# Performance work log

Hardware: AMD Instinct MI355X
Metric: run time of the kernel (lower is better)

Reference implementation:

```python
import jax, jax.numpy as jnp
import numpy as np
import math

B, H, S, D = 4, 16, 2048, 64

def setup_inputs() -> dict:
    key = jax.random.key(0)
    kq, kk, kv, km = jax.random.split(key, 4)
    query = jax.random.normal(kq, (B, H, S, D), dtype=jnp.float32)
    k = jax.random.normal(kk, (B, H, S, D), dtype=jnp.float32)
    value = jax.random.normal(kv, (B, H, S, D), dtype=jnp.float32)
    mask = jax.random.randint(km, (1, 1, S, S), 0, 2) == 1  # True = masked
    return {"query": query, "key": k, "value": value, "mask": mask}

def reference(query, key, value, mask):
    # scores: [B,H,S,S]
    scale = 1.0 / math.sqrt(key.shape[-1])
    scores = jnp.einsum('bhqd,bhkd->bhqk', query, key) * scale
    scores = jnp.where(mask, -jnp.inf, scores)
    probs = jax.nn.softmax(scores, axis=-1)
    out = jnp.einsum('bhqk,bhkd->bhqd', probs, value)
    return out
```

## Files before the change

### kernel.cpp

```cpp
#include <hip/hip_runtime.h>
#include <hip/hip_bf16.h>
#include <stdint.h>

#define BHN 64
#define SEQ 2048
#define DH  64

typedef unsigned short u16;
typedef __attribute__((ext_vector_type(8))) short bf16x8;
typedef __attribute__((ext_vector_type(16))) float f32x16;

__device__ inline u16 f2bf(float x){
  union { float f; uint32_t u; } a; a.f = x;
  uint32_t u = a.u;
  uint32_t lsb = (u >> 16) & 1u;
  u += 0x7FFFu + lsb;
  return (u16)(u >> 16);
}

__device__ inline float fast_exp2(float x){
#if __has_builtin(__builtin_amdgcn_exp2f)
  return __builtin_amdgcn_exp2f(x);
#else
  float r; asm("v_exp_f32 %0, %1" : "=v"(r) : "v"(x)); return r;
#endif
}

__device__ inline void gload_lds16(const void* g, void* l){
  __builtin_amdgcn_global_load_lds(
      (const __attribute__((address_space(1))) void*)g,
      (__attribute__((address_space(3))) void*)l, 16, 0, 0);
}


__global__ __launch_bounds__(256) void build_tiles(const float* __restrict__ kf,
                                                   const float* __restrict__ vf,
                                                   u16* __restrict__ tiles){
  __shared__ float sVf[64][65];
  int head = blockIdx.x >> 5;
  int kt   = blockIdx.x & 31;
  int k0   = kt * 64;
  int t = threadIdx.x;

  {
    int r = t >> 2;
    int dseg = (t & 3) * 16;
    const float* src = vf + ((int64_t)(head*SEQ + k0 + r))*DH + dseg;
    #pragma unroll
    for (int j = 0; j < 16; j += 4){
      float4 v = *(const float4*)(src + j);
      sVf[r][dseg+j+0] = v.x; sVf[r][dseg+j+1] = v.y;
      sVf[r][dseg+j+2] = v.z; sVf[r][dseg+j+3] = v.w;
    }
  }

  u16* outb = tiles + ((size_t)(head*32 + kt) << 13);

  #pragma unroll
  for (int i = 0; i < 2; i++){
    int cid = i*256 + t;
    int f = cid >> 6;
    int l = cid & 63;
    int kh = f >> 2, ds = f & 3;
    int row = k0 + kh*32 + (l & 31);
    int dstart = ds*16 + (l >> 5)*8;
    const float* src = kf + ((int64_t)(head*SEQ + row))*DH + dstart;
    float4 a = *(const float4*)(src);
    float4 b = *(const float4*)(src + 4);
    union { u16 h[8]; uint4 v; } pk;
    pk.h[0]=f2bf(a.x); pk.h[1]=f2bf(a.y); pk.h[2]=f2bf(a.z); pk.h[3]=f2bf(a.w);
    pk.h[4]=f2bf(b.x); pk.h[5]=f2bf(b.y); pk.h[6]=f2bf(b.z); pk.h[7]=f2bf(b.w);
    *(uint4*)(outb + f*512 + l*8) = pk.v;
  }

  __syncthreads();

  #pragma unroll
  for (int i = 0; i < 2; i++){
    int cid = i*256 + t;
    int g = cid >> 6;
    int l = cid & 63;
    int oh = g >> 2, ks = g & 3;
    int d  = oh*32 + (l & 31);
    int kk = ks*16 + (l >> 5)*8;
    union { u16 h[8]; uint4 v; } pk;
    #pragma unroll
    for (int j = 0; j < 8; j++) pk.h[j] = f2bf(sVf[kk+j][d]);
    *(uint4*)(outb + (8+g)*512 + l*8) = pk.v;
  }
}

__global__ __launch_bounds__(256) void pack_mask(const void* __restrict__ mraw,
                                                 uint32_t* __restrict__ mkp){
  __shared__ int sflag;
  int t = threadIdx.x;
  const uint32_t* m32 = (const uint32_t*)mraw;
  if (t == 0) sflag = 0;
  __syncthreads();
  if (t < 64){
    uint32_t v = m32[t] | m32[t+64] | m32[t+128] | m32[t+192];
    if (v > 1u) atomicOr(&sflag, 1);
  }
  __syncthreads();
  bool isbool = (sflag != 0);
  int idx = blockIdx.x*256 + t;
  int row = idx >> 6;
  int wd  = idx & 63;
  uint32_t bits = 0;
  if (isbool){
    const uint8_t* mb = (const uint8_t*)mraw + (int64_t)row*SEQ + wd*32;
    uint4 a = ((const uint4*)mb)[0];
    uint4 b = ((const uint4*)mb)[1];
    uint32_t words[8] = {a.x,a.y,a.z,a.w,b.x,b.y,b.z,b.w};
    #pragma unroll
    for (int i = 0; i < 32; i++){
      int kl = (i&3) + 8*((i>>2)&3) + 4*(i>>4);
      uint32_t byte = (words[kl>>2] >> (8*(kl&3))) & 0xFFu;
      bits |= (byte ? 0u : 1u) << i;
    }
  } else {
    const uint32_t* mi = m32 + (int64_t)row*SEQ + wd*32;
    uint32_t words[32];
    #pragma unroll
    for (int j = 0; j < 32; j += 4){
      uint4 v = *(const uint4*)(mi + j);
      words[j+0]=v.x; words[j+1]=v.y; words[j+2]=v.z; words[j+3]=v.w;
    }
    #pragma unroll
    for (int i = 0; i < 32; i++){
      int kl = (i&3) + 8*((i>>2)&3) + 4*(i>>4);
      bits |= (words[kl] ? 0u : 1u) << i;
    }
  }
  mkp[((size_t)(wd >> 1)*SEQ + row)*2 + (wd & 1)] = bits;
}


__global__ __launch_bounds__(256, 4) void attn_mfma(
    const float* __restrict__ qf, const u16* __restrict__ tiles,
    const uint32_t* __restrict__ mkp, float* __restrict__ out)
{
  __shared__ __align__(16) char lds[2*16384 + 512];

  int bid = blockIdx.x;
  int logical = (bid & 7)*128 + (bid >> 3);
  int head = logical >> 4;
  int q0   = (logical & 15) * 128;

  int t  = threadIdx.x;
  int w  = t >> 6;
  int l  = t & 63;
  int l31 = l & 31;
  int hi  = l >> 5;
  int hi16 = hi << 4;

  const float QS = 0.125f * 1.4426950408889634f;
  bf16x8 qfr[4];
  {
    const float* qrow = qf + ((size_t)(head*SEQ + q0 + w*32 + l31))*DH + hi*8;
    #pragma unroll
    for (int ds = 0; ds < 4; ds++){
      float4 a = *(const float4*)(qrow + ds*16);
      float4 b = *(const float4*)(qrow + ds*16 + 4);
      uint32_t u0, u1, u2, u3;
      asm("v_cvt_pk_bf16_f32 %0, %1, %2" : "=v"(u0) : "v"(a.x*QS), "v"(a.y*QS));
      asm("v_cvt_pk_bf16_f32 %0, %1, %2" : "=v"(u1) : "v"(a.z*QS), "v"(a.w*QS));
      asm("v_cvt_pk_bf16_f32 %0, %1, %2" : "=v"(u2) : "v"(b.x*QS), "v"(b.y*QS));
      asm("v_cvt_pk_bf16_f32 %0, %1, %2" : "=v"(u3) : "v"(b.z*QS), "v"(b.w*QS));
      union { uint32_t u[4]; bf16x8 h; } pk_;
      pk_.u[0]=u0; pk_.u[1]=u1; pk_.u[2]=u2; pk_.u[3]=u3;
      qfr[ds] = pk_.h;
    }
  }

  const uint2* mptr = (const uint2*)mkp + (q0 + w*32 + l31);

  const char* tb = (const char*)tiles + ((size_t)head << 19) + w*4096 + l*16;
  char* dwave = lds + w*4096;

  f32x16 O0 = {0,0,0,0,0,0,0,0,0,0,0,0,0,0,0,0};
  f32x16 O1 = {0,0,0,0,0,0,0,0,0,0,0,0,0,0,0,0};
  float ls0 = 0.f, ls1 = 0.f;

  const char* ldsL = lds + l*16;

  auto STAGE = [&](int kt64, int bufoff){
    const char* s_ = tb + ((size_t)kt64 << 14);
    char* d_ = dwave + bufoff;
    gload_lds16(s_,        d_);
    gload_lds16(s_ + 1024, d_ + 1024);
    gload_lds16(s_ + 2048, d_ + 2048);
    gload_lds16(s_ + 3072, d_ + 3072);
  };

  STAGE(0, 0);
  uint2 mw2 = *mptr; mptr += SEQ;
  __syncthreads();

  int cur = 0;
  for (int kt = 0; kt < 32; kt++){
    uint2 mw2n = mw2;
    if (kt < 31){
      STAGE(kt+1, cur ^ 16384);
      mw2n = *mptr; mptr += SEQ;
    }

    const char* lb = ldsL + cur;

    #pragma unroll
    for (int g = 0; g < 2; g++){
      uint32_t wsh = (g ? mw2.y : mw2.x) >> hi16;

      f32x16 c = {0,0,0,0,0,0,0,0,0,0,0,0,0,0,0,0};
      __builtin_amdgcn_s_setprio(1);
      #pragma unroll
      for (int ds = 0; ds < 4; ds++){
        bf16x8 kfr = *(const bf16x8*)(lb + (4*g + ds)*1024);
        c = __builtin_amdgcn_mfma_f32_32x32x16_bf16(kfr, qfr[ds], c, 0, 0, 0);
      }
      __builtin_amdgcn_s_setprio(0);

      float p[16];
      #pragma unroll
      for (int r = 0; r < 16; r++){
        float pe = fast_exp2(c[r]);
        int32_t km;
        asm("v_bfe_i32 %0, %1, %2, 1" : "=v"(km) : "v"(wsh), "n"(r));
        p[r] = __uint_as_float(__float_as_uint(pe) & (uint32_t)km);
      }
      #pragma unroll
      for (int r = 0; r < 8; r++){ ls0 += p[r]; ls1 += p[r+8]; }

      bf16x8 pa0, pa1;
      {
        uint32_t A0, A1, B0, B1;
        asm("v_cvt_pk_bf16_f32 %0, %1, %2" : "=v"(A0) : "v"(p[0]), "v"(p[1]));
        asm("v_cvt_pk_bf16_f32 %0, %1, %2" : "=v"(A1) : "v"(p[2]), "v"(p[3]));
        asm("v_cvt_pk_bf16_f32 %0, %1, %2" : "=v"(B0) : "v"(p[4]), "v"(p[5]));
        asm("v_cvt_pk_bf16_f32 %0, %1, %2" : "=v"(B1) : "v"(p[6]), "v"(p[7]));
        asm("v_permlane32_swap_b32 %0, %1" : "+v"(A0), "+v"(B0));
        asm("v_permlane32_swap_b32 %0, %1" : "+v"(A1), "+v"(B1));
        union { uint32_t u[4]; bf16x8 h; } pk_;
        pk_.u[0] = A0; pk_.u[1] = A1; pk_.u[2] = B0; pk_.u[3] = B1;
        pa0 = pk_.h;
      }
      {
        uint32_t A0, A1, B0, B1;
        asm("v_cvt_pk_bf16_f32 %0, %1, %2" : "=v"(A0) : "v"(p[8]),  "v"(p[9]));
        asm("v_cvt_pk_bf16_f32 %0, %1, %2" : "=v"(A1) : "v"(p[10]), "v"(p[11]));
        asm("v_cvt_pk_bf16_f32 %0, %1, %2" : "=v"(B0) : "v"(p[12]), "v"(p[13]));
        asm("v_cvt_pk_bf16_f32 %0, %1, %2" : "=v"(B1) : "v"(p[14]), "v"(p[15]));
        asm("v_permlane32_swap_b32 %0, %1" : "+v"(A0), "+v"(B0));
        asm("v_permlane32_swap_b32 %0, %1" : "+v"(A1), "+v"(B1));
        union { uint32_t u[4]; bf16x8 h; } pk_;
        pk_.u[0] = A0; pk_.u[1] = A1; pk_.u[2] = B0; pk_.u[3] = B1;
        pa1 = pk_.h;
      }

      __builtin_amdgcn_s_setprio(1);
      {
        bf16x8 v00 = *(const bf16x8*)(lb + (8  + 2*g)*1024);
        bf16x8 v01 = *(const bf16x8*)(lb + (9  + 2*g)*1024);
        bf16x8 v10 = *(const bf16x8*)(lb + (12 + 2*g)*1024);
        bf16x8 v11 = *(const bf16x8*)(lb + (13 + 2*g)*1024);
        O0 = __builtin_amdgcn_mfma_f32_32x32x16_bf16(pa0, v00, O0, 0, 0, 0);
        O0 = __builtin_amdgcn_mfma_f32_32x32x16_bf16(pa1, v01, O0, 0, 0, 0);
        O1 = __builtin_amdgcn_mfma_f32_32x32x16_bf16(pa0, v10, O1, 0, 0, 0);
        O1 = __builtin_amdgcn_mfma_f32_32x32x16_bf16(pa1, v11, O1, 0, 0, 0);
      }
      __builtin_amdgcn_s_setprio(0);
    }

    mw2 = mw2n;
    __syncthreads();
    cur ^= 16384;
  }

  float lt = ls0 + ls1;
  {
    uint32_t a = __float_as_uint(lt), b = a;
    asm("v_permlane32_swap_b32 %0, %1" : "+v"(a), "+v"(b));
    lt = __uint_as_float(a) + __uint_as_float(b);
  }
  float* sInv = (float*)(lds + 32768);
  if (hi == 0) sInv[w*32 + l31] = 1.0f / lt;
  float* obase = out + ((size_t)(head*SEQ + q0 + w*32))*DH + l31;
  #pragma unroll
  for (int r = 0; r < 16; r++){
    int qr = (r&3) + 8*(r>>2) + 4*hi;
    float inv = sInv[w*32 + qr];
    obase[(size_t)qr*DH]      = O0[r] * inv;
    obase[(size_t)qr*DH + 32] = O1[r] * inv;
  }
}


__global__ __launch_bounds__(256) void attn_naive(
    const float* __restrict__ qf, const float* __restrict__ kf,
    const float* __restrict__ vf, const void* __restrict__ mraw,
    float* __restrict__ out)
{
  __shared__ float sq[64];
  __shared__ float sS[SEQ];
  __shared__ float redM[4], redS[4];
  __shared__ float sO[4][64];
  __shared__ int sflag;

  int bid = blockIdx.x;
  int bh = bid >> 11;
  int q  = bid & 2047;
  int t  = threadIdx.x;
  const uint32_t* m32 = (const uint32_t*)mraw;
  if (t == 0) sflag = 0;
  __syncthreads();
  if (t < 64){
    uint32_t v = m32[t] | m32[t+64] | m32[t+128] | m32[t+192];
    if (v > 1u) atomicOr(&sflag, 1);
  }
  if (t < 64) sq[t] = qf[((int64_t)bh*SEQ + q)*DH + t] * (0.125f*1.4426950408889634f);
  __syncthreads();
  bool isbool = (sflag != 0);

  float lmax = -3e38f;
  for (int k = t; k < SEQ; k += 256){
    bool masked = isbool ? (((const uint8_t*)mraw)[(int64_t)q*SEQ + k] != 0)
                         : (m32[(int64_t)q*SEQ + k] != 0);
    float s = -3e38f;
    if (!masked){
      const float* krow = kf + ((int64_t)bh*SEQ + k)*DH;
      float acc = 0.f;
      for (int d = 0; d < 64; d++) acc += sq[d]*krow[d];
      s = acc;
    }
    sS[k] = s;
    lmax = fmaxf(lmax, s);
  }
  for (int o = 32; o >= 1; o >>= 1) lmax = fmaxf(lmax, __shfl_xor(lmax, o));
  if ((t & 63) == 0) redM[t >> 6] = lmax;
  __syncthreads();
  float m = fmaxf(fmaxf(redM[0], redM[1]), fmaxf(redM[2], redM[3]));
  float lsum = 0.f;
  for (int k = t; k < SEQ; k += 256){
    float p = exp2f(sS[k] - m);
    sS[k] = p;
    lsum += p;
  }
  for (int o = 32; o >= 1; o >>= 1) lsum += __shfl_xor(lsum, o);
  if ((t & 63) == 0) redS[t >> 6] = lsum;
  __syncthreads();
  float lden = redS[0] + redS[1] + redS[2] + redS[3];

  float o = 0.f;
  int d = t & 63;
  int c = t >> 6;
  for (int k = c*512; k < (c+1)*512; k++)
    o += sS[k] * vf[((int64_t)bh*SEQ + k)*DH + d];
  sO[c][d] = o;
  __syncthreads();
  if (t < 64){
    float r = (sO[0][t] + sO[1][t] + sO[2][t] + sO[3][t]) / lden;
    out[((int64_t)bh*SEQ + q)*DH + t] = r;
  }
}


extern "C" void kernel_launch(void* const* d_in, const int* in_sizes, int n_in,
                              void* d_out, int out_size, void* d_ws, size_t ws_size,
                              hipStream_t stream)
{
  const float* qf = (const float*)d_in[0];
  const float* kf = (const float*)d_in[1];
  const float* vf = (const float*)d_in[2];
  const void*  mraw = d_in[3];
  float* out = (float*)d_out;

  size_t tilesB = (size_t)BHN*32*16384;
  size_t need = tilesB + (size_t)SEQ*64*4 + 256;
  if (ws_size >= need){
    u16* tiles = (u16*)d_ws;
    uint32_t* mkp = (uint32_t*)((char*)d_ws + tilesB);
    hipLaunchKernelGGL(build_tiles, dim3(2048), dim3(256), 0, stream, kf, vf, tiles);
    hipLaunchKernelGGL(pack_mask,   dim3(512),  dim3(256), 0, stream, mraw, mkp);
    hipLaunchKernelGGL(attn_mfma,   dim3(1024), dim3(256), 0, stream, qf, tiles, mkp, out);
  } else {
    hipLaunchKernelGGL(attn_naive, dim3(BHN*SEQ), dim3(256), 0, stream, qf, kf, vf, mraw, out);
  }
}
```

Measured before the change: 112.3 us.

## Fold mask into MFMA accumulator init, sum rows via MFMA, relax barriers

The score accumulator now starts at -128 for masked positions and 0 otherwise, so the QK MFMA adds the mask bias and the per-element bitmask AND after exp2 goes away. Row sums are produced by two extra MFMAs per group against a vector of bf16 ones, replacing the scalar adds, the cross-lane reduction and the LDS reciprocal buffer. The __syncthreads calls become an explicit vmcnt wait plus raw s_barrier, with prefetch issued unconditionally (the last iteration reloads a tile it does not need). The trade-off is more MFMA work per tile in exchange for fewer VALU ops, and masking now relies on exp2 of a -128 bias underflowing to near zero.

```diff
diff --git a/kernel.cpp b/kernel.cpp
--- a/kernel.cpp
+++ b/kernel.cpp
@@ -140,7 +140,7 @@
     const float* __restrict__ qf, const u16* __restrict__ tiles,
     const uint32_t* __restrict__ mkp, float* __restrict__ out)
 {
-  __shared__ __align__(16) char lds[2*16384 + 512];
+  __shared__ __align__(16) char lds[2*16384];
 
   int bid = blockIdx.x;
   int logical = (bid & 7)*128 + (bid >> 3);
@@ -173,14 +173,21 @@
     }
   }
 
-  const uint2* mptr = (const uint2*)mkp + (q0 + w*32 + l31);
+  bf16x8 ones;
+  {
+    union { uint32_t u[4]; bf16x8 h; } o_;
+    o_.u[0]=o_.u[1]=o_.u[2]=o_.u[3]=0x3F803F80u;
+    ones = o_.h;
+  }
+
+  const uint2* mbase = (const uint2*)mkp + (q0 + w*32 + l31);
 
   const char* tb = (const char*)tiles + ((size_t)head << 19) + w*4096 + l*16;
   char* dwave = lds + w*4096;
 
-  f32x16 O0 = {0,0,0,0,0,0,0,0,0,0,0,0,0,0,0,0};
-  f32x16 O1 = {0,0,0,0,0,0,0,0,0,0,0,0,0,0,0,0};
-  float ls0 = 0.f, ls1 = 0.f;
+  f32x16 O0   = {0,0,0,0,0,0,0,0,0,0,0,0,0,0,0,0};
+  f32x16 O1   = {0,0,0,0,0,0,0,0,0,0,0,0,0,0,0,0};
+  f32x16 Osum = {0,0,0,0,0,0,0,0,0,0,0,0,0,0,0,0};
 
   const char* ldsL = lds + l*16;
 
@@ -194,24 +201,35 @@
   };
 
   STAGE(0, 0);
-  uint2 mw2 = *mptr; mptr += SEQ;
-  __syncthreads();
+  asm volatile("" ::: "memory");
+  uint2 mw2 = *mbase;
 
   int cur = 0;
+  #pragma unroll 1
   for (int kt = 0; kt < 32; kt++){
-    uint2 mw2n = mw2;
-    if (kt < 31){
-      STAGE(kt+1, cur ^ 16384);
-      mw2n = *mptr; mptr += SEQ;
-    }
+    int nt = (kt < 31) ? (kt + 1) : 31;
+    STAGE(nt, cur ^ 16384);
+    asm volatile("" ::: "memory");
+    uint2 mnext = mbase[(size_t)nt*SEQ];
+
+    asm volatile("s_waitcnt vmcnt(6)" ::: "memory");
+    __builtin_amdgcn_s_barrier();
+    asm volatile("" ::: "memory");
 
     const char* lb = ldsL + cur;
 
     #pragma unroll
     for (int g = 0; g < 2; g++){
-      uint32_t wsh = (g ? mw2.y : mw2.x) >> hi16;
-
-      f32x16 c = {0,0,0,0,0,0,0,0,0,0,0,0,0,0,0,0};
+      uint32_t nsh = ~((g ? mw2.y : mw2.x) >> hi16);
+
+      f32x16 c;
+      #pragma unroll
+      for (int r = 0; r < 16; r++){
+        int32_t km;
+        asm("v_bfe_i32 %0, %1, %2, 1" : "=v"(km) : "v"(nsh), "n"(r));
+        c[r] = __uint_as_float((uint32_t)km & 0xC3000000u);
+      }
+
       __builtin_amdgcn_s_setprio(1);
       #pragma unroll
       for (int ds = 0; ds < 4; ds++){
@@ -222,14 +240,7 @@
 
       float p[16];
       #pragma unroll
-      for (int r = 0; r < 16; r++){
-        float pe = fast_exp2(c[r]);
-        int32_t km;
-        asm("v_bfe_i32 %0, %1, %2, 1" : "=v"(km) : "v"(wsh), "n"(r));
-        p[r] = __uint_as_float(__float_as_uint(pe) & (uint32_t)km);
-      }
-      #pragma unroll
-      for (int r = 0; r < 8; r++){ ls0 += p[r]; ls1 += p[r+8]; }
+      for (int r = 0; r < 16; r++) p[r] = fast_exp2(c[r]);
 
       bf16x8 pa0, pa1;
       {
@@ -263,32 +274,29 @@
         bf16x8 v01 = *(const bf16x8*)(lb + (9  + 2*g)*1024);
         bf16x8 v10 = *(const bf16x8*)(lb + (12 + 2*g)*1024);
         bf16x8 v11 = *(const bf16x8*)(lb + (13 + 2*g)*1024);
-        O0 = __builtin_amdgcn_mfma_f32_32x32x16_bf16(pa0, v00, O0, 0, 0, 0);
-        O0 = __builtin_amdgcn_mfma_f32_32x32x16_bf16(pa1, v01, O0, 0, 0, 0);
-        O1 = __builtin_amdgcn_mfma_f32_32x32x16_bf16(pa0, v10, O1, 0, 0, 0);
-        O1 = __builtin_amdgcn_mfma_f32_32x32x16_bf16(pa1, v11, O1, 0, 0, 0);
+        O0   = __builtin_amdgcn_mfma_f32_32x32x16_bf16(pa0, v00, O0, 0, 0, 0);
+        O0   = __builtin_amdgcn_mfma_f32_32x32x16_bf16(pa1, v01, O0, 0, 0, 0);
+        O1   = __builtin_amdgcn_mfma_f32_32x32x16_bf16(pa0, v10, O1, 0, 0, 0);
+        O1   = __builtin_amdgcn_mfma_f32_32x32x16_bf16(pa1, v11, O1, 0, 0, 0);
+        Osum = __builtin_amdgcn_mfma_f32_32x32x16_bf16(pa0, ones, Osum, 0, 0, 0);
+        Osum = __builtin_amdgcn_mfma_f32_32x32x16_bf16(pa1, ones, Osum, 0, 0, 0);
       }
       __builtin_amdgcn_s_setprio(0);
     }
 
-    mw2 = mw2n;
-    __syncthreads();
+    asm volatile("" ::: "memory");
+    __builtin_amdgcn_s_barrier();
+    asm volatile("" ::: "memory");
+
+    mw2 = mnext;
     cur ^= 16384;
   }
 
-  float lt = ls0 + ls1;
-  {
-    uint32_t a = __float_as_uint(lt), b = a;
-    asm("v_permlane32_swap_b32 %0, %1" : "+v"(a), "+v"(b));
-    lt = __uint_as_float(a) + __uint_as_float(b);
-  }
-  float* sInv = (float*)(lds + 32768);
-  if (hi == 0) sInv[w*32 + l31] = 1.0f / lt;
   float* obase = out + ((size_t)(head*SEQ + q0 + w*32))*DH + l31;
   #pragma unroll
   for (int r = 0; r < 16; r++){
     int qr = (r&3) + 8*(r>>2) + 4*hi;
-    float inv = sInv[w*32 + qr];
+    float inv = 1.0f / Osum[r];
     obase[(size_t)qr*DH]      = O0[r] * inv;
     obase[(size_t)qr*DH + 32] = O1[r] * inv;
   }
```

After: 114.0 us. No clear change (+1.5%).

## Fold mask into MFMA accumulator init and interleave both score tiles with waitcnt pipelining

Applied to the files above, without the earlier changes.

The mask is no longer applied after exp2. Each score accumulator is seeded with a large negative bias (0xC3000000, about -128) for masked positions, so exp2 underflows to zero and the per-element AND after the exponent goes away. The two QK^T MFMA chains now issue back to back before the softmax and PV stages, so the second tile's MFMAs overlap the first tile's exp. __syncthreads is replaced by an explicit vmcnt wait and raw barriers, with unconditional prefetch (the last tile is reloaded redundantly). This risks correctness if the -128 bias does not fully zero a masked entry, and it raises register pressure from holding two accumulators.

```diff
diff --git a/kernel.cpp b/kernel.cpp
--- a/kernel.cpp
+++ b/kernel.cpp
@@ -173,7 +173,7 @@
     }
   }
 
-  const uint2* mptr = (const uint2*)mkp + (q0 + w*32 + l31);
+  const uint2* mbase = (const uint2*)mkp + (q0 + w*32 + l31);
 
   const char* tb = (const char*)tiles + ((size_t)head << 19) + w*4096 + l*16;
   char* dwave = lds + w*4096;
@@ -193,86 +193,122 @@
     gload_lds16(s_ + 3072, d_ + 3072);
   };
 
+  auto SMPACK = [&](f32x16& c, bf16x8& pa0, bf16x8& pa1){
+    float p[16];
+    #pragma unroll
+    for (int r = 0; r < 16; r++) p[r] = fast_exp2(c[r]);
+    #pragma unroll
+    for (int r = 0; r < 8; r++){ ls0 += p[r]; ls1 += p[r+8]; }
+    {
+      uint32_t A0, A1, B0, B1;
+      asm("v_cvt_pk_bf16_f32 %0, %1, %2" : "=v"(A0) : "v"(p[0]), "v"(p[1]));
+      asm("v_cvt_pk_bf16_f32 %0, %1, %2" : "=v"(A1) : "v"(p[2]), "v"(p[3]));
+      asm("v_cvt_pk_bf16_f32 %0, %1, %2" : "=v"(B0) : "v"(p[4]), "v"(p[5]));
+      asm("v_cvt_pk_bf16_f32 %0, %1, %2" : "=v"(B1) : "v"(p[6]), "v"(p[7]));
+      asm("v_permlane32_swap_b32 %0, %1" : "+v"(A0), "+v"(B0));
+      asm("v_permlane32_swap_b32 %0, %1" : "+v"(A1), "+v"(B1));
+      union { uint32_t u[4]; bf16x8 h; } pk_;
+      pk_.u[0] = A0; pk_.u[1] = A1; pk_.u[2] = B0; pk_.u[3] = B1;
+      pa0 = pk_.h;
+    }
+    {
+      uint32_t A0, A1, B0, B1;
+      asm("v_cvt_pk_bf16_f32 %0, %1, %2" : "=v"(A0) : "v"(p[8]),  "v"(p[9]));
+      asm("v_cvt_pk_bf16_f32 %0, %1, %2" : "=v"(A1) : "v"(p[10]), "v"(p[11]));
+      asm("v_cvt_pk_bf16_f32 %0, %1, %2" : "=v"(B0) : "v"(p[12]), "v"(p[13]));
+      asm("v_cvt_pk_bf16_f32 %0, %1, %2" : "=v"(B1) : "v"(p[14]), "v"(p[15]));
+      asm("v_permlane32_swap_b32 %0, %1" : "+v"(A0), "+v"(B0));
+      asm("v_permlane32_swap_b32 %0, %1" : "+v"(A1), "+v"(B1));
+      union { uint32_t u[4]; bf16x8 h; } pk_;
+      pk_.u[0] = A0; pk_.u[1] = A1; pk_.u[2] = B0; pk_.u[3] = B1;
+      pa1 = pk_.h;
+    }
+  };
+
   STAGE(0, 0);
-  uint2 mw2 = *mptr; mptr += SEQ;
-  __syncthreads();
+  asm volatile("" ::: "memory");
+  uint2 mw2 = *mbase;
 
   int cur = 0;
+  #pragma unroll 1
   for (int kt = 0; kt < 32; kt++){
-    uint2 mw2n = mw2;
-    if (kt < 31){
-      STAGE(kt+1, cur ^ 16384);
-      mw2n = *mptr; mptr += SEQ;
-    }
+    int nt = (kt < 31) ? (kt + 1) : 31;
+    STAGE(nt, cur ^ 16384);
+    asm volatile("" ::: "memory");
+    uint2 mnext = mbase[(size_t)nt*SEQ];
+
+    asm volatile("s_waitcnt vmcnt(6)" ::: "memory");
+    __builtin_amdgcn_s_barrier();
+    asm volatile("" ::: "memory");
 
     const char* lb = ldsL + cur;
-
-    #pragma unroll
-    for (int g = 0; g < 2; g++){
-      uint32_t wsh = (g ? mw2.y : mw2.x) >> hi16;
-
-      f32x16 c = {0,0,0,0,0,0,0,0,0,0,0,0,0,0,0,0};
-      __builtin_amdgcn_s_setprio(1);
-      #pragma unroll
-      for (int ds = 0; ds < 4; ds++){
-        bf16x8 kfr = *(const bf16x8*)(lb + (4*g + ds)*1024);
-        c = __builtin_amdgcn_mfma_f32_32x32x16_bf16(kfr, qfr[ds], c, 0, 0, 0);
-      }
-      __builtin_amdgcn_s_setprio(0);
-
-      float p[16];
-      #pragma unroll
-      for (int r = 0; r < 16; r++){
-        float pe = fast_exp2(c[r]);
-        int32_t km;
-        asm("v_bfe_i32 %0, %1, %2, 1" : "=v"(km) : "v"(wsh), "n"(r));
-        p[r] = __uint_as_float(__float_as_uint(pe) & (uint32_t)km);
-      }
-      #pragma unroll
-      for (int r = 0; r < 8; r++){ ls0 += p[r]; ls1 += p[r+8]; }
-
-      bf16x8 pa0, pa1;
-      {
-        uint32_t A0, A1, B0, B1;
-        asm("v_cvt_pk_bf16_f32 %0, %1, %2" : "=v"(A0) : "v"(p[0]), "v"(p[1]));
-        asm("v_cvt_pk_bf16_f32 %0, %1, %2" : "=v"(A1) : "v"(p[2]), "v"(p[3]));
-        asm("v_cvt_pk_bf16_f32 %0, %1, %2" : "=v"(B0) : "v"(p[4]), "v"(p[5]));
-        asm("v_cvt_pk_bf16_f32 %0, %1, %2" : "=v"(B1) : "v"(p[6]), "v"(p[7]));
-        asm("v_permlane32_swap_b32 %0, %1" : "+v"(A0), "+v"(B0));
-        asm("v_permlane32_swap_b32 %0, %1" : "+v"(A1), "+v"(B1));
-        union { uint32_t u[4]; bf16x8 h; } pk_;
-        pk_.u[0] = A0; pk_.u[1] = A1; pk_.u[2] = B0; pk_.u[3] = B1;
-        pa0 = pk_.h;
-      }
-      {
-        uint32_t A0, A1, B0, B1;
-        asm("v_cvt_pk_bf16_f32 %0, %1, %2" : "=v"(A0) : "v"(p[8]),  "v"(p[9]));
-        asm("v_cvt_pk_bf16_f32 %0, %1, %2" : "=v"(A1) : "v"(p[10]), "v"(p[11]));
-        asm("v_cvt_pk_bf16_f32 %0, %1, %2" : "=v"(B0) : "v"(p[12]), "v"(p[13]));
-        asm("v_cvt_pk_bf16_f32 %0, %1, %2" : "=v"(B1) : "v"(p[14]), "v"(p[15]));
-        asm("v_permlane32_swap_b32 %0, %1" : "+v"(A0), "+v"(B0));
-        asm("v_permlane32_swap_b32 %0, %1" : "+v"(A1), "+v"(B1));
-        union { uint32_t u[4]; bf16x8 h; } pk_;
-        pk_.u[0] = A0; pk_.u[1] = A1; pk_.u[2] = B0; pk_.u[3] = B1;
-        pa1 = pk_.h;
-      }
-
-      __builtin_amdgcn_s_setprio(1);
-      {
-        bf16x8 v00 = *(const bf16x8*)(lb + (8  + 2*g)*1024);
-        bf16x8 v01 = *(const bf16x8*)(lb + (9  + 2*g)*1024);
-        bf16x8 v10 = *(const bf16x8*)(lb + (12 + 2*g)*1024);
-        bf16x8 v11 = *(const bf16x8*)(lb + (13 + 2*g)*1024);
-        O0 = __builtin_amdgcn_mfma_f32_32x32x16_bf16(pa0, v00, O0, 0, 0, 0);
-        O0 = __builtin_amdgcn_mfma_f32_32x32x16_bf16(pa1, v01, O0, 0, 0, 0);
-        O1 = __builtin_amdgcn_mfma_f32_32x32x16_bf16(pa0, v10, O1, 0, 0, 0);
-        O1 = __builtin_amdgcn_mfma_f32_32x32x16_bf16(pa1, v11, O1, 0, 0, 0);
-      }
-      __builtin_amdgcn_s_setprio(0);
-    }
-
-    mw2 = mw2n;
-    __syncthreads();
+    uint32_t nsh0 = ~(mw2.x >> hi16);
+    uint32_t nsh1 = ~(mw2.y >> hi16);
+
+    f32x16 c0, c1;
+    #pragma unroll
+    for (int r = 0; r < 16; r++){
+      int32_t km;
+      asm("v_bfe_i32 %0, %1, %2, 1" : "=v"(km) : "v"(nsh0), "n"(r));
+      c0[r] = __uint_as_float((uint32_t)km & 0xC3000000u);
+    }
+    #pragma unroll
+    for (int r = 0; r < 16; r++){
+      int32_t km;
+      asm("v_bfe_i32 %0, %1, %2, 1" : "=v"(km) : "v"(nsh1), "n"(r));
+      c1[r] = __uint_as_float((uint32_t)km & 0xC3000000u);
+    }
+
+    __builtin_amdgcn_s_setprio(1);
+    #pragma unroll
+    for (int ds = 0; ds < 4; ds++){
+      bf16x8 kfr = *(const bf16x8*)(lb + ds*1024);
+      c0 = __builtin_amdgcn_mfma_f32_32x32x16_bf16(kfr, qfr[ds], c0, 0, 0, 0);
+    }
+    #pragma unroll
+    for (int ds = 0; ds < 4; ds++){
+      bf16x8 kfr = *(const bf16x8*)(lb + (4 + ds)*1024);
+      c1 = __builtin_amdgcn_mfma_f32_32x32x16_bf16(kfr, qfr[ds], c1, 0, 0, 0);
+    }
+    __builtin_amdgcn_s_setprio(0);
+
+    bf16x8 pa0, pa1;
+    SMPACK(c0, pa0, pa1);
+
+    __builtin_amdgcn_s_setprio(1);
+    {
+      bf16x8 v00 = *(const bf16x8*)(lb + 8*1024);
+      bf16x8 v01 = *(const bf16x8*)(lb + 9*1024);
+      bf16x8 v10 = *(const bf16x8*)(lb + 12*1024);
+      bf16x8 v11 = *(const bf16x8*)(lb + 13*1024);
+      O0 = __builtin_amdgcn_mfma_f32_32x32x16_bf16(pa0, v00, O0, 0, 0, 0);
+      O0 = __builtin_amdgcn_mfma_f32_32x32x16_bf16(pa1, v01, O0, 0, 0, 0);
+      O1 = __builtin_amdgcn_mfma_f32_32x32x16_bf16(pa0, v10, O1, 0, 0, 0);
+      O1 = __builtin_amdgcn_mfma_f32_32x32x16_bf16(pa1, v11, O1, 0, 0, 0);
+    }
+    __builtin_amdgcn_s_setprio(0);
+
+    bf16x8 pb0, pb1;
+    SMPACK(c1, pb0, pb1);
+
+    __builtin_amdgcn_s_setprio(1);
+    {
+      bf16x8 v00 = *(const bf16x8*)(lb + 10*1024);
+      bf16x8 v01 = *(const bf16x8*)(lb + 11*1024);
+      bf16x8 v10 = *(const bf16x8*)(lb + 14*1024);
+      bf16x8 v11 = *(const bf16x8*)(lb + 15*1024);
+      O0 = __builtin_amdgcn_mfma_f32_32x32x16_bf16(pb0, v00, O0, 0, 0, 0);
+      O0 = __builtin_amdgcn_mfma_f32_32x32x16_bf16(pb1, v01, O0, 0, 0, 0);
+      O1 = __builtin_amdgcn_mfma_f32_32x32x16_bf16(pb0, v10, O1, 0, 0, 0);
+      O1 = __builtin_amdgcn_mfma_f32_32x32x16_bf16(pb1, v11, O1, 0, 0, 0);
+    }
+    __builtin_amdgcn_s_setprio(0);
+
+    asm volatile("" ::: "memory");
+    __builtin_amdgcn_s_barrier();
+    asm volatile("" ::: "memory");
+
+    mw2 = mnext;
     cur ^= 16384;
   }
 
```

After: 112.3 us. No clear change (-0.0%).

## Merge prepass kernels and pipeline K/V staging with partial waitcnt barriers

Applied to the files above, without the earlier changes.

The tile-build and mask-pack kernels are fused into one prepass launch, which removes a kernel launch. In the attention kernel, the per-iteration __syncthreads is replaced by an s_waitcnt vmcnt(5) plus raw s_barrier, so the next tile's global-to-LDS loads stay in flight while the current tile is computed. The kernel also drops the LDS used for the inverse row sums in favor of ds_bpermute and reuses the MFMA accumulator for probabilities. Launch bounds are raised to 5 waves for occupancy. The hand-tuned vmcnt count and the redundant staging on the last iteration carry a correctness and ordering risk.

```diff
diff --git a/kernel.cpp b/kernel.cpp
--- a/kernel.cpp
+++ b/kernel.cpp
@@ -33,114 +33,114 @@
 }
 
 
-__global__ __launch_bounds__(256) void build_tiles(const float* __restrict__ kf,
-                                                   const float* __restrict__ vf,
-                                                   u16* __restrict__ tiles){
-  __shared__ float sVf[64][65];
-  int head = blockIdx.x >> 5;
-  int kt   = blockIdx.x & 31;
-  int k0   = kt * 64;
+__global__ __launch_bounds__(256) void prepass(const float* __restrict__ kf,
+                                               const float* __restrict__ vf,
+                                               const void* __restrict__ mraw,
+                                               u16* __restrict__ tiles,
+                                               uint32_t* __restrict__ mkp){
   int t = threadIdx.x;
-
-  {
-    int r = t >> 2;
-    int dseg = (t & 3) * 16;
-    const float* src = vf + ((int64_t)(head*SEQ + k0 + r))*DH + dseg;
+  if (blockIdx.x < 2048){
+    __shared__ float sVf[64][65];
+    int head = blockIdx.x >> 5;
+    int kt   = blockIdx.x & 31;
+    int k0   = kt * 64;
+
+    {
+      int r = t >> 2;
+      int dseg = (t & 3) * 16;
+      const float* src = vf + ((int64_t)(head*SEQ + k0 + r))*DH + dseg;
+      #pragma unroll
+      for (int j = 0; j < 16; j += 4){
+        float4 v = *(const float4*)(src + j);
+        sVf[r][dseg+j+0] = v.x; sVf[r][dseg+j+1] = v.y;
+        sVf[r][dseg+j+2] = v.z; sVf[r][dseg+j+3] = v.w;
+      }
+    }
+
+    u16* outb = tiles + ((size_t)(head*32 + kt) << 13);
+
     #pragma unroll
-    for (int j = 0; j < 16; j += 4){
-      float4 v = *(const float4*)(src + j);
-      sVf[r][dseg+j+0] = v.x; sVf[r][dseg+j+1] = v.y;
-      sVf[r][dseg+j+2] = v.z; sVf[r][dseg+j+3] = v.w;
-    }
-  }
-
-  u16* outb = tiles + ((size_t)(head*32 + kt) << 13);
-
-  #pragma unroll
-  for (int i = 0; i < 2; i++){
-    int cid = i*256 + t;
-    int f = cid >> 6;
-    int l = cid & 63;
-    int kh = f >> 2, ds = f & 3;
-    int row = k0 + kh*32 + (l & 31);
-    int dstart = ds*16 + (l >> 5)*8;
-    const float* src = kf + ((int64_t)(head*SEQ + row))*DH + dstart;
-    float4 a = *(const float4*)(src);
-    float4 b = *(const float4*)(src + 4);
-    union { u16 h[8]; uint4 v; } pk;
-    pk.h[0]=f2bf(a.x); pk.h[1]=f2bf(a.y); pk.h[2]=f2bf(a.z); pk.h[3]=f2bf(a.w);
-    pk.h[4]=f2bf(b.x); pk.h[5]=f2bf(b.y); pk.h[6]=f2bf(b.z); pk.h[7]=f2bf(b.w);
-    *(uint4*)(outb + f*512 + l*8) = pk.v;
-  }
-
-  __syncthreads();
-
-  #pragma unroll
-  for (int i = 0; i < 2; i++){
-    int cid = i*256 + t;
-    int g = cid >> 6;
-    int l = cid & 63;
-    int oh = g >> 2, ks = g & 3;
-    int d  = oh*32 + (l & 31);
-    int kk = ks*16 + (l >> 5)*8;
-    union { u16 h[8]; uint4 v; } pk;
+    for (int i = 0; i < 2; i++){
+      int cid = i*256 + t;
+      int f = cid >> 6;
+      int l = cid & 63;
+      int kh = f >> 2, ds = f & 3;
+      int row = k0 + kh*32 + (l & 31);
+      int dstart = ds*16 + (l >> 5)*8;
+      const float* src = kf + ((int64_t)(head*SEQ + row))*DH + dstart;
+      float4 a = *(const float4*)(src);
+      float4 b = *(const float4*)(src + 4);
+      union { u16 h[8]; uint4 v; } pk;
+      pk.h[0]=f2bf(a.x); pk.h[1]=f2bf(a.y); pk.h[2]=f2bf(a.z); pk.h[3]=f2bf(a.w);
+      pk.h[4]=f2bf(b.x); pk.h[5]=f2bf(b.y); pk.h[6]=f2bf(b.z); pk.h[7]=f2bf(b.w);
+      *(uint4*)(outb + f*512 + l*8) = pk.v;
+    }
+
+    __syncthreads();
+
     #pragma unroll
-    for (int j = 0; j < 8; j++) pk.h[j] = f2bf(sVf[kk+j][d]);
-    *(uint4*)(outb + (8+g)*512 + l*8) = pk.v;
-  }
-}
-
-__global__ __launch_bounds__(256) void pack_mask(const void* __restrict__ mraw,
-                                                 uint32_t* __restrict__ mkp){
-  __shared__ int sflag;
-  int t = threadIdx.x;
-  const uint32_t* m32 = (const uint32_t*)mraw;
-  if (t == 0) sflag = 0;
-  __syncthreads();
-  if (t < 64){
-    uint32_t v = m32[t] | m32[t+64] | m32[t+128] | m32[t+192];
-    if (v > 1u) atomicOr(&sflag, 1);
-  }
-  __syncthreads();
-  bool isbool = (sflag != 0);
-  int idx = blockIdx.x*256 + t;
-  int row = idx >> 6;
-  int wd  = idx & 63;
-  uint32_t bits = 0;
-  if (isbool){
-    const uint8_t* mb = (const uint8_t*)mraw + (int64_t)row*SEQ + wd*32;
-    uint4 a = ((const uint4*)mb)[0];
-    uint4 b = ((const uint4*)mb)[1];
-    uint32_t words[8] = {a.x,a.y,a.z,a.w,b.x,b.y,b.z,b.w};
-    #pragma unroll
-    for (int i = 0; i < 32; i++){
-      int kl = (i&3) + 8*((i>>2)&3) + 4*(i>>4);
-      uint32_t byte = (words[kl>>2] >> (8*(kl&3))) & 0xFFu;
-      bits |= (byte ? 0u : 1u) << i;
+    for (int i = 0; i < 2; i++){
+      int cid = i*256 + t;
+      int g = cid >> 6;
+      int l = cid & 63;
+      int oh = g >> 2, ks = g & 3;
+      int d  = oh*32 + (l & 31);
+      int kk = ks*16 + (l >> 5)*8;
+      union { u16 h[8]; uint4 v; } pk;
+      #pragma unroll
+      for (int j = 0; j < 8; j++) pk.h[j] = f2bf(sVf[kk+j][d]);
+      *(uint4*)(outb + (8+g)*512 + l*8) = pk.v;
     }
   } else {
-    const uint32_t* mi = m32 + (int64_t)row*SEQ + wd*32;
-    uint32_t words[32];
-    #pragma unroll
-    for (int j = 0; j < 32; j += 4){
-      uint4 v = *(const uint4*)(mi + j);
-      words[j+0]=v.x; words[j+1]=v.y; words[j+2]=v.z; words[j+3]=v.w;
-    }
-    #pragma unroll
-    for (int i = 0; i < 32; i++){
-      int kl = (i&3) + 8*((i>>2)&3) + 4*(i>>4);
-      bits |= (words[kl] ? 0u : 1u) << i;
-    }
-  }
-  mkp[((size_t)(wd >> 1)*SEQ + row)*2 + (wd & 1)] = bits;
-}
-
-
-__global__ __launch_bounds__(256, 4) void attn_mfma(
+    __shared__ int sflag;
+    const uint32_t* m32 = (const uint32_t*)mraw;
+    if (t == 0) sflag = 0;
+    __syncthreads();
+    if (t < 64){
+      uint32_t v = m32[t] | m32[t+64] | m32[t+128] | m32[t+192];
+      if (v > 1u) atomicOr(&sflag, 1);
+    }
+    __syncthreads();
+    bool isbool = (sflag != 0);
+    int idx = (blockIdx.x - 2048)*256 + t;
+    int row = idx >> 6;
+    int wd  = idx & 63;
+    uint32_t bits = 0;
+    if (isbool){
+      const uint8_t* mb = (const uint8_t*)mraw + (int64_t)row*SEQ + wd*32;
+      uint4 a = ((const uint4*)mb)[0];
+      uint4 b = ((const uint4*)mb)[1];
+      uint32_t words[8] = {a.x,a.y,a.z,a.w,b.x,b.y,b.z,b.w};
+      #pragma unroll
+      for (int i = 0; i < 32; i++){
+        int kl = (i&3) + 8*((i>>2)&3) + 4*(i>>4);
+        uint32_t byte = (words[kl>>2] >> (8*(kl&3))) & 0xFFu;
+        bits |= (byte ? 0u : 1u) << i;
+      }
+    } else {
+      const uint32_t* mi = m32 + (int64_t)row*SEQ + wd*32;
+      uint32_t words[32];
+      #pragma unroll
+      for (int j = 0; j < 32; j += 4){
+        uint4 v = *(const uint4*)(mi + j);
+        words[j+0]=v.x; words[j+1]=v.y; words[j+2]=v.z; words[j+3]=v.w;
+      }
+      #pragma unroll
+      for (int i = 0; i < 32; i++){
+        int kl = (i&3) + 8*((i>>2)&3) + 4*(i>>4);
+        bits |= (words[kl] ? 0u : 1u) << i;
+      }
+    }
+    mkp[((size_t)(wd >> 1)*SEQ + row)*2 + (wd & 1)] = bits;
+  }
+}
+
+
+__global__ __launch_bounds__(256, 5) void attn_mfma(
     const float* __restrict__ qf, const u16* __restrict__ tiles,
     const uint32_t* __restrict__ mkp, float* __restrict__ out)
 {
-  __shared__ __align__(16) char lds[2*16384 + 512];
+  __shared__ __align__(16) char lds[2*16384];
 
   int bid = blockIdx.x;
   int logical = (bid & 7)*128 + (bid >> 3);
@@ -173,7 +173,7 @@
     }
   }
 
-  const uint2* mptr = (const uint2*)mkp + (q0 + w*32 + l31);
+  const uint2* mbase = (const uint2*)mkp + (q0 + w*32 + l31);
 
   const char* tb = (const char*)tiles + ((size_t)head << 19) + w*4096 + l*16;
   char* dwave = lds + w*4096;
@@ -194,16 +194,20 @@
   };
 
   STAGE(0, 0);
-  uint2 mw2 = *mptr; mptr += SEQ;
-  __syncthreads();
+  asm volatile("" ::: "memory");
+  uint2 mw2 = *mbase;
 
   int cur = 0;
+  #pragma unroll 1
   for (int kt = 0; kt < 32; kt++){
-    uint2 mw2n = mw2;
-    if (kt < 31){
-      STAGE(kt+1, cur ^ 16384);
-      mw2n = *mptr; mptr += SEQ;
-    }
+    int nt = (kt < 31) ? (kt + 1) : 31;
+    STAGE(nt, cur ^ 16384);
+    asm volatile("" ::: "memory");
+    uint2 mnext = mbase[(size_t)nt*SEQ];
+
+    asm volatile("s_waitcnt vmcnt(5)" ::: "memory");
+    __builtin_amdgcn_s_barrier();
+    asm volatile("" ::: "memory");
 
     const char* lb = ldsL + cur;
 
@@ -220,24 +224,23 @@
       }
       __builtin_amdgcn_s_setprio(0);
 
-      float p[16];
       #pragma unroll
       for (int r = 0; r < 16; r++){
         float pe = fast_exp2(c[r]);
         int32_t km;
         asm("v_bfe_i32 %0, %1, %2, 1" : "=v"(km) : "v"(wsh), "n"(r));
-        p[r] = __uint_as_float(__float_as_uint(pe) & (uint32_t)km);
-      }
-      #pragma unroll
-      for (int r = 0; r < 8; r++){ ls0 += p[r]; ls1 += p[r+8]; }
+        c[r] = __uint_as_float(__float_as_uint(pe) & (uint32_t)km);
+      }
+      #pragma unroll
+      for (int r = 0; r < 8; r++){ ls0 += c[r]; ls1 += c[r+8]; }
 
       bf16x8 pa0, pa1;
       {
         uint32_t A0, A1, B0, B1;
-        asm("v_cvt_pk_bf16_f32 %0, %1, %2" : "=v"(A0) : "v"(p[0]), "v"(p[1]));
-        asm("v_cvt_pk_bf16_f32 %0, %1, %2" : "=v"(A1) : "v"(p[2]), "v"(p[3]));
-        asm("v_cvt_pk_bf16_f32 %0, %1, %2" : "=v"(B0) : "v"(p[4]), "v"(p[5]));
-        asm("v_cvt_pk_bf16_f32 %0, %1, %2" : "=v"(B1) : "v"(p[6]), "v"(p[7]));
+        asm("v_cvt_pk_bf16_f32 %0, %1, %2" : "=v"(A0) : "v"(c[0]), "v"(c[1]));
+        asm("v_cvt_pk_bf16_f32 %0, %1, %2" : "=v"(A1) : "v"(c[2]), "v"(c[3]));
+        asm("v_cvt_pk_bf16_f32 %0, %1, %2" : "=v"(B0) : "v"(c[4]), "v"(c[5]));
+        asm("v_cvt_pk_bf16_f32 %0, %1, %2" : "=v"(B1) : "v"(c[6]), "v"(c[7]));
         asm("v_permlane32_swap_b32 %0, %1" : "+v"(A0), "+v"(B0));
         asm("v_permlane32_swap_b32 %0, %1" : "+v"(A1), "+v"(B1));
         union { uint32_t u[4]; bf16x8 h; } pk_;
@@ -246,10 +249,10 @@
       }
       {
         uint32_t A0, A1, B0, B1;
-        asm("v_cvt_pk_bf16_f32 %0, %1, %2" : "=v"(A0) : "v"(p[8]),  "v"(p[9]));
-        asm("v_cvt_pk_bf16_f32 %0, %1, %2" : "=v"(A1) : "v"(p[10]), "v"(p[11]));
-        asm("v_cvt_pk_bf16_f32 %0, %1, %2" : "=v"(B0) : "v"(p[12]), "v"(p[13]));
-        asm("v_cvt_pk_bf16_f32 %0, %1, %2" : "=v"(B1) : "v"(p[14]), "v"(p[15]));
+        asm("v_cvt_pk_bf16_f32 %0, %1, %2" : "=v"(A0) : "v"(c[8]),  "v"(c[9]));
+        asm("v_cvt_pk_bf16_f32 %0, %1, %2" : "=v"(A1) : "v"(c[10]), "v"(c[11]));
+        asm("v_cvt_pk_bf16_f32 %0, %1, %2" : "=v"(B0) : "v"(c[12]), "v"(c[13]));
+        asm("v_cvt_pk_bf16_f32 %0, %1, %2" : "=v"(B1) : "v"(c[14]), "v"(c[15]));
         asm("v_permlane32_swap_b32 %0, %1" : "+v"(A0), "+v"(B0));
         asm("v_permlane32_swap_b32 %0, %1" : "+v"(A1), "+v"(B1));
         union { uint32_t u[4]; bf16x8 h; } pk_;
@@ -271,8 +274,11 @@
       __builtin_amdgcn_s_setprio(0);
     }
 
-    mw2 = mw2n;
-    __syncthreads();
+    asm volatile("" ::: "memory");
+    __builtin_amdgcn_s_barrier();
+    asm volatile("" ::: "memory");
+
+    mw2 = mnext;
     cur ^= 16384;
   }
 
@@ -282,15 +288,17 @@
     asm("v_permlane32_swap_b32 %0, %1" : "+v"(a), "+v"(b));
     lt = __uint_as_float(a) + __uint_as_float(b);
   }
-  float* sInv = (float*)(lds + 32768);
-  if (hi == 0) sInv[w*32 + l31] = 1.0f / lt;
+  float inv = 1.0f / lt;
   float* obase = out + ((size_t)(head*SEQ + q0 + w*32))*DH + l31;
   #pragma unroll
   for (int r = 0; r < 16; r++){
-    int qr = (r&3) + 8*(r>>2) + 4*hi;
-    float inv = sInv[w*32 + qr];
-    obase[(size_t)qr*DH]      = O0[r] * inv;
-    obase[(size_t)qr*DH + 32] = O1[r] * inv;
+    int qrb = (r&3) + 8*(r>>2);
+    int invr_i = __builtin_amdgcn_ds_bpermute((qrb << 2) + hi16,
+                                              (int)__float_as_uint(inv));
+    float invr = __uint_as_float((uint32_t)invr_i);
+    int qr = qrb + 4*hi;
+    obase[(size_t)qr*DH]      = O0[r] * invr;
+    obase[(size_t)qr*DH + 32] = O1[r] * invr;
   }
 }
 
@@ -379,9 +387,8 @@
   if (ws_size >= need){
     u16* tiles = (u16*)d_ws;
     uint32_t* mkp = (uint32_t*)((char*)d_ws + tilesB);
-    hipLaunchKernelGGL(build_tiles, dim3(2048), dim3(256), 0, stream, kf, vf, tiles);
-    hipLaunchKernelGGL(pack_mask,   dim3(512),  dim3(256), 0, stream, mraw, mkp);
-    hipLaunchKernelGGL(attn_mfma,   dim3(1024), dim3(256), 0, stream, qf, tiles, mkp, out);
+    hipLaunchKernelGGL(prepass,   dim3(2560), dim3(256), 0, stream, kf, vf, mraw, tiles, mkp);
+    hipLaunchKernelGGL(attn_mfma, dim3(1024), dim3(256), 0, stream, qf, tiles, mkp, out);
   } else {
     hipLaunchKernelGGL(attn_naive, dim3(BHN*SEQ), dim3(256), 0, stream, qf, kf, vf, mraw, out);
   }
```

Result: slower. 119.3 us (+6.3%).
